# Performance work log

Measured on AMD Instinct MI355X. Metric: run time of the kernel, lower is better.

The kernel has to match this reference:

```python
import jax, jax.numpy as jnp
import numpy as np

B, S, D = 2, 4096, 1024
H, DK = 16, 64          # heads, QK feature dim per head
DV = D // H             # output features per head = 64
QKV_OUT = (2 * DK + DV) * H  # 3072


def setup_inputs() -> dict:
    key = jax.random.key(0)
    k1, k2, k3, k4, k5 = jax.random.split(key, 5)
    x = jax.random.normal(k1, (B, S, D), dtype=jnp.float32)
    Wqkv = jax.random.normal(k2, (D, QKV_OUT), dtype=jnp.float32) * (1.0 / np.sqrt(D))
    bqkv = jnp.zeros((QKV_OUT,), dtype=jnp.float32)
    Wproj = jax.random.normal(k3, (D, D), dtype=jnp.float32) * (1.0 / np.sqrt(D))
    bproj = jnp.zeros((D,), dtype=jnp.float32)
    return {"x": x, "Wqkv": Wqkv, "bqkv": bqkv, "Wproj": Wproj, "bproj": bproj}


def reference(x, Wqkv, bqkv, Wproj, bproj):
    # QKV projection: [B,S,(2*DK+DV)*H]
    qkv = x @ Wqkv + bqkv
    q_len = DK * H
    Q = qkv[:, :, :q_len].reshape(B, S, H, DK).transpose(0, 2, 1, 3)        # [B,H,S,DK]
    K = qkv[:, :, q_len:2 * q_len].reshape(B, S, H, DK).transpose(0, 2, 1, 3)
    V = qkv[:, :, 2 * q_len:].reshape(B, S, H, DV).transpose(0, 2, 1, 3)    # [B,H,S,DV]

    scores = jnp.einsum("bhqd,bhkd->bhqk", Q, K) * (1.0 / np.sqrt(DK))
    # Faithful to source: causal mask is tril(ones) with zeros -> -inf,
    # i.e. +1.0 is ADDED on allowed positions (harmless constant shift per row).
    tril = jnp.tril(jnp.ones((S, S), dtype=jnp.float32))
    mask = jnp.where(tril == 0, -jnp.inf, tril)
    scores = scores + mask
    attn = jax.nn.softmax(scores, axis=-1)  # dropout disabled (p=0 / eval)

    out = jnp.einsum("bhqk,bhkd->bhqd", attn, V)            # [B,H,S,DV]
    out = out.transpose(0, 2, 1, 3).reshape(B, S, H * DV)   # [B,S,D]
    return out @ Wproj + bproj
```

## Files before the change

kernel.cpp:

```cpp
#include <hip/hip_runtime.h>
#include <stdint.h>


typedef __bf16 bf16x8 __attribute__((ext_vector_type(8)));
typedef float f32x4 __attribute__((ext_vector_type(4)));
typedef unsigned short u16x8 __attribute__((ext_vector_type(8)));
typedef unsigned short u16x4 __attribute__((ext_vector_type(4)));
typedef unsigned int u32x4 __attribute__((ext_vector_type(4)));

__device__ __forceinline__ unsigned short f2bf(float f) {
  unsigned u = __builtin_bit_cast(unsigned, f);
  u += 0x7FFFu + ((u >> 16) & 1u);
  return (unsigned short)(u >> 16);
}

__device__ __forceinline__ float fast_exp2(float x) {
#if __has_builtin(__builtin_amdgcn_exp2f)
  return __builtin_amdgcn_exp2f(x);
#else
  return exp2f(x);
#endif
}

__device__ __forceinline__ void gload16(const void* g, void* l) {
  __builtin_amdgcn_global_load_lds(
      (__attribute__((address_space(1))) unsigned int*)(uintptr_t)g,
      (__attribute__((address_space(3))) unsigned int*)(unsigned int)(uintptr_t)l,
      16, 0, 0);
}

__global__ void k_cvt_bf16(const float* __restrict__ in,
                           unsigned short* __restrict__ out, int n8) {
  int i = blockIdx.x * blockDim.x + threadIdx.x;
  if (i >= n8) return;
  const float4* p = reinterpret_cast<const float4*>(in) + (size_t)i * 2;
  float4 a = p[0], b = p[1];
  u16x8 o;
  o[0] = f2bf(a.x); o[1] = f2bf(a.y); o[2] = f2bf(a.z); o[3] = f2bf(a.w);
  o[4] = f2bf(b.x); o[5] = f2bf(b.y); o[6] = f2bf(b.z); o[7] = f2bf(b.w);
  *(reinterpret_cast<u16x8*>(out) + i) = o;
}

__global__ void k_transcvt(const float* __restrict__ in,
                           unsigned short* __restrict__ out, int K, int N) {
  __shared__ float tile[32][33];
  int tk0 = blockIdx.y << 5, tn0 = blockIdx.x << 5;
  int t = threadIdx.x;
  int r = t >> 3, c4 = (t & 7) << 2;
  float4 v = *reinterpret_cast<const float4*>(&in[(size_t)(tk0 + r) * N + tn0 + c4]);
  tile[r][c4 + 0] = v.x; tile[r][c4 + 1] = v.y;
  tile[r][c4 + 2] = v.z; tile[r][c4 + 3] = v.w;
  __syncthreads();
  u16x4 o;
  o[0] = f2bf(tile[c4 + 0][r]); o[1] = f2bf(tile[c4 + 1][r]);
  o[2] = f2bf(tile[c4 + 2][r]); o[3] = f2bf(tile[c4 + 3][r]);
  *reinterpret_cast<u16x4*>(&out[(size_t)(tn0 + r) * K + tk0 + c4]) = o;
}

__global__ __launch_bounds__(512, 2) void k_gemm_qkv256(
    const unsigned short* __restrict__ A, const unsigned short* __restrict__ Bt,
    const float* __restrict__ bias, unsigned short* __restrict__ Qb,
    unsigned short* __restrict__ Kb, unsigned short* __restrict__ VTb) {
  __shared__ unsigned short Aring[4][8192];
  __shared__ unsigned short Bring[4][8192];
  const int t = threadIdx.x;
  const int lane = t & 63;
  const int w = t >> 6;
  const int wr = w >> 2, wc = w & 3;
  const int l15 = lane & 15, l4 = lane >> 4;
  const int m0 = blockIdx.y << 8, n0 = blockIdx.x << 8;

  const int ca0 = t, ca1 = t + 512;
  const size_t gA0 = (size_t)(m0 + (ca0 & 255)) * 1024 + ((ca0 >> 8) << 3);
  const size_t gA1 = (size_t)(m0 + (ca1 & 255)) * 1024 + ((ca1 >> 8) << 3);
  const size_t gB0 = (size_t)(n0 + (ca0 & 255)) * 1024 + ((ca0 >> 8) << 3);
  const size_t gB1 = (size_t)(n0 + (ca1 & 255)) * 1024 + ((ca1 >> 8) << 3);

  const int abase = l4 * 2048 + (wr * 128 + l15) * 8;
  const int bbase = l4 * 2048 + (wc * 64 + l15) * 8;

  f32x4 acc[8][4] = {};

  auto stageU = [&](int g) {
    const int s = g & 3;
    const int k = g << 5;
    gload16(A + gA0 + k, &Aring[s][ca0 * 8]);
    gload16(A + gA1 + k, &Aring[s][ca1 * 8]);
    gload16(Bt + gB0 + k, &Bring[s][ca0 * 8]);
    gload16(Bt + gB1 + k, &Bring[s][ca1 * 8]);
  };

  auto computeU = [&](int g, bool doStage) {
    const unsigned short* As = Aring[g & 3];
    const unsigned short* Bs = Bring[g & 3];
    bf16x8 bfr[4], af[4];
#pragma unroll
    for (int nf = 0; nf < 4; ++nf)
      bfr[nf] = *reinterpret_cast<const bf16x8*>(Bs + bbase + nf * 128);
#pragma unroll
    for (int mf = 0; mf < 4; ++mf)
      af[mf] = *reinterpret_cast<const bf16x8*>(As + abase + mf * 128);
    if (doStage) stageU(g + 3);
    __builtin_amdgcn_s_setprio(1);
#pragma unroll
    for (int mf = 0; mf < 4; ++mf)
#pragma unroll
      for (int nf = 0; nf < 4; ++nf)
        acc[mf][nf] = __builtin_amdgcn_mfma_f32_16x16x32_bf16(af[mf], bfr[nf],
                                                              acc[mf][nf], 0, 0, 0);
    __builtin_amdgcn_s_setprio(0);
#pragma unroll
    for (int mf = 0; mf < 4; ++mf)
      af[mf] = *reinterpret_cast<const bf16x8*>(As + abase + 512 + mf * 128);
    __builtin_amdgcn_s_setprio(1);
#pragma unroll
    for (int mf = 0; mf < 4; ++mf)
#pragma unroll
      for (int nf = 0; nf < 4; ++nf)
        acc[4 + mf][nf] = __builtin_amdgcn_mfma_f32_16x16x32_bf16(
            af[mf], bfr[nf], acc[4 + mf][nf], 0, 0, 0);
    __builtin_amdgcn_s_setprio(0);
  };

  stageU(0); stageU(1); stageU(2);
  asm volatile("s_waitcnt vmcnt(8)" ::: "memory");
  asm volatile("s_barrier" ::: "memory");

#pragma unroll 1
  for (int g = 0; g < 29; ++g) {
    computeU(g, true);
    asm volatile("s_waitcnt vmcnt(8)" ::: "memory");
    asm volatile("s_barrier" ::: "memory");
  }
  computeU(29, false);
  asm volatile("s_waitcnt vmcnt(4)" ::: "memory");
  asm volatile("s_barrier" ::: "memory");
  computeU(30, false);
  asm volatile("s_waitcnt vmcnt(0)" ::: "memory");
  asm volatile("s_barrier" ::: "memory");
  computeU(31, false);

  const float C1 = 0.18033688011112043f;
  float bi[4];
#pragma unroll
  for (int nf = 0; nf < 4; ++nf) bi[nf] = bias[n0 + wc * 64 + nf * 16 + l15];

  if (n0 < 1024) {
#pragma unroll
    for (int amf = 0; amf < 8; ++amf)
#pragma unroll
      for (int nf = 0; nf < 4; ++nf)
#pragma unroll
        for (int j = 0; j < 4; ++j) {
          int row = m0 + wr * 128 + amf * 16 + l4 * 4 + j;
          int col = n0 + wc * 64 + nf * 16 + l15;
          float v = (acc[amf][nf][j] + bi[nf]) * C1;
          int b = row >> 12, s = row & 4095;
          int hh = col >> 6, d = col & 63;
          Qb[((size_t)(b * 16 + hh) * 4096 + s) * 64 + d] = f2bf(v);
        }
  } else if (n0 < 2048) {
#pragma unroll
    for (int amf = 0; amf < 8; ++amf)
#pragma unroll
      for (int nf = 0; nf < 4; ++nf)
#pragma unroll
        for (int j = 0; j < 4; ++j) {
          int row = m0 + wr * 128 + amf * 16 + l4 * 4 + j;
          int cc = n0 - 1024 + wc * 64 + nf * 16 + l15;
          float v = acc[amf][nf][j] + bi[nf];
          int b = row >> 12, s = row & 4095;
          int hh = cc >> 6, d = cc & 63;
          Kb[((size_t)(b * 16 + hh) * 4096 + s) * 64 + d] = f2bf(v);
        }
  } else {
#pragma unroll
    for (int amf = 0; amf < 8; ++amf)
#pragma unroll
      for (int nf = 0; nf < 4; ++nf)
#pragma unroll
        for (int j = 0; j < 4; ++j) {
          int row = m0 + wr * 128 + amf * 16 + l4 * 4 + j;
          int cc = n0 - 2048 + wc * 64 + nf * 16 + l15;
          float v = acc[amf][nf][j] + bi[nf];
          int b = row >> 12, s = row & 4095;
          int hh = cc >> 6, d = cc & 63;
          VTb[((size_t)(b * 16 + hh) * 64 + d) * 4096 + s] = f2bf(v);
        }
  }
}

__device__ __forceinline__ void gemm_core(
    const unsigned short* __restrict__ A, const unsigned short* __restrict__ Bt,
    unsigned short* Al, unsigned short* Bl, int m0, int n0, f32x4 acc[4][4]) {
  const int t = threadIdx.x;
  const int lane = t & 63;
  const int w = t >> 6;
  const int wr = w >> 1, wc = w & 1;
  const int l15 = lane & 15, l4 = lane >> 4;

  const int c0 = t, c1 = t + 256;
  const int r0 = c0 >> 2, s0 = ((c0 & 3) << 3) ^ (((r0 >> 1) & 3) << 3);
  const int r1 = c1 >> 2, s1 = ((c1 & 3) << 3) ^ (((r1 >> 1) & 3) << 3);
  const size_t ga0 = (size_t)(m0 + r0) * 1024 + s0;
  const size_t ga1 = (size_t)(m0 + r1) * 1024 + s1;
  const size_t gb0 = (size_t)(n0 + r0) * 1024 + s0;
  const size_t gb1 = (size_t)(n0 + r1) * 1024 + s1;

  int aidx[4], bidx[4];
#pragma unroll
  for (int m = 0; m < 4; ++m) {
    int row = wr * 64 + m * 16 + l15;
    aidx[m] = row * 32 + ((l4 * 8) ^ (((row >> 1) & 3) << 3));
    row = wc * 64 + m * 16 + l15;
    bidx[m] = row * 32 + ((l4 * 8) ^ (((row >> 1) & 3) << 3));
  }

  for (int kk = 0; kk < 1024; kk += 32) {
    __syncthreads();
    gload16(A + ga0 + kk, Al + c0 * 8);
    gload16(A + ga1 + kk, Al + c1 * 8);
    gload16(Bt + gb0 + kk, Bl + c0 * 8);
    gload16(Bt + gb1 + kk, Bl + c1 * 8);
    __syncthreads();
    bf16x8 af[4], bfr[4];
#pragma unroll
    for (int m = 0; m < 4; ++m)
      af[m] = *reinterpret_cast<const bf16x8*>(Al + aidx[m]);
#pragma unroll
    for (int n = 0; n < 4; ++n)
      bfr[n] = *reinterpret_cast<const bf16x8*>(Bl + bidx[n]);
#pragma unroll
    for (int m = 0; m < 4; ++m)
#pragma unroll
      for (int n = 0; n < 4; ++n)
        acc[m][n] = __builtin_amdgcn_mfma_f32_16x16x32_bf16(af[m], bfr[n],
                                                            acc[m][n], 0, 0, 0);
  }
}

__global__ __launch_bounds__(256) void k_gemm_proj(
    const unsigned short* __restrict__ A, const unsigned short* __restrict__ Bt,
    const float* __restrict__ bias, float* __restrict__ out) {
  __shared__ unsigned short Al[128 * 32];
  __shared__ unsigned short Bl[128 * 32];
  const int lane = threadIdx.x & 63, w = threadIdx.x >> 6;
  const int wr = w >> 1, wc = w & 1;
  const int l15 = lane & 15, l4 = lane >> 4;
  const int m0 = blockIdx.y << 7, n0 = blockIdx.x << 7;

  f32x4 acc[4][4] = {};
  gemm_core(A, Bt, Al, Bl, m0, n0, acc);

#pragma unroll
  for (int m = 0; m < 4; ++m) {
#pragma unroll
    for (int n = 0; n < 4; ++n) {
#pragma unroll
      for (int j = 0; j < 4; ++j) {
        int row = m0 + wr * 64 + m * 16 + l4 * 4 + j;
        int col = n0 + wc * 64 + n * 16 + l15;
        out[(size_t)row * 1024 + col] = acc[m][n][j] + bias[col];
      }
    }
  }
}

__global__ __launch_bounds__(256, 4) void k_attn(
    const unsigned short* __restrict__ Qb, const unsigned short* __restrict__ Kb,
    const unsigned short* __restrict__ VTb, unsigned short* __restrict__ Ob) {
  __shared__ unsigned short Kl[2][64 * 64];
  __shared__ unsigned short Vl[2][64 * 64];
  const int t = threadIdx.x;
  const int lane = t & 63, w = t >> 6;
  const int l15 = lane & 15, l4 = lane >> 4;
  const int idx = blockIdx.x;
  const int qt = 31 - (idx >> 5);
  const int bh = idx & 31;
  const size_t qkbase = (size_t)bh * 4096 * 64;
  const size_t vbase = (size_t)bh * 64 * 4096;
  const int b = bh >> 4, hh = bh & 15;
  const int wrow0 = qt * 128 + w * 32;
  const int nt = 2 * qt + 2;

  const int c0 = t, c1 = t + 256;
  const int kr0 = c0 >> 3, ks0 = ((c0 & 7) << 3) ^ ((kr0 & 7) << 3);
  const int kr1 = c1 >> 3, ks1 = ((c1 & 7) << 3) ^ ((kr1 & 7) << 3);

#define STAGE(bufi, jt)                                                             \
  do {                                                                              \
    gload16(Kb + qkbase + (size_t)((jt) * 64 + kr0) * 64 + ks0, &Kl[bufi][c0 * 8]); \
    gload16(Kb + qkbase + (size_t)((jt) * 64 + kr1) * 64 + ks1, &Kl[bufi][c1 * 8]); \
    gload16(VTb + vbase + (size_t)kr0 * 4096 + (jt) * 64 + ks0, &Vl[bufi][c0 * 8]); \
    gload16(VTb + vbase + (size_t)kr1 * 4096 + (jt) * 64 + ks1, &Vl[bufi][c1 * 8]); \
  } while (0)

  bf16x8 qf[2][2];
#pragma unroll
  for (int m = 0; m < 2; ++m)
#pragma unroll
    for (int kk = 0; kk < 2; ++kk)
      qf[m][kk] = *reinterpret_cast<const bf16x8*>(
          &Qb[qkbase + (size_t)(wrow0 + m * 16 + l15) * 64 + kk * 32 + l4 * 8]);

  f32x4 oacc[2][4] = {};
  float lsum[2] = {};

  STAGE(0, 0);
  asm volatile("s_waitcnt vmcnt(0)" ::: "memory");
  __builtin_amdgcn_s_barrier();

  for (int j = 0; j < nt; ++j) {
    const int cur = j & 1;
    if (j + 1 < nt) STAGE(cur ^ 1, j + 1);

    const int jk0 = j * 64;
    const bool active = (jk0 <= wrow0 + 31);
    const bool needmask = active && (jk0 + 63 > wrow0);

    if (active) {
#pragma unroll
      for (int h = 0; h < 2; ++h) {
        f32x4 sch[2][2] = {};
        __builtin_amdgcn_s_setprio(1);
#pragma unroll
        for (int nn = 0; nn < 2; ++nn) {
          int krow = (h * 2 + nn) * 16 + l15;
#pragma unroll
          for (int kk = 0; kk < 2; ++kk) {
            int kcol = (kk * 32 + l4 * 8) ^ ((krow & 7) << 3);
            bf16x8 kfr = *reinterpret_cast<const bf16x8*>(&Kl[cur][krow * 64 + kcol]);
#pragma unroll
            for (int m = 0; m < 2; ++m)
              sch[m][nn] = __builtin_amdgcn_mfma_f32_16x16x32_bf16(
                  kfr, qf[m][kk], sch[m][nn], 0, 0, 0);
          }
        }
        __builtin_amdgcn_s_setprio(0);

        bf16x8 pa[2];
#pragma unroll
        for (int m = 0; m < 2; ++m) {
#pragma unroll
          for (int nn = 0; nn < 2; ++nn)
#pragma unroll
            for (int r = 0; r < 4; ++r)
              sch[m][nn][r] = fast_exp2(sch[m][nn][r]);
          if (needmask) {
            const int qg = wrow0 + m * 16 + l15;
#pragma unroll
            for (int nn = 0; nn < 2; ++nn) {
              const int kb = jk0 + (h * 2 + nn) * 16 + l4 * 4;
#pragma unroll
              for (int r = 0; r < 4; ++r)
                if (kb + r > qg) sch[m][nn][r] = 0.f;
            }
          }
#pragma unroll
          for (int nn = 0; nn < 2; ++nn)
#pragma unroll
            for (int r = 0; r < 4; ++r)
              lsum[m] += sch[m][nn][r];

          unsigned A0, A1, B0, B1;
          asm("v_cvt_pk_bf16_f32 %0, %1, %2"
              : "=v"(A0) : "v"(sch[m][0][0]), "v"(sch[m][0][1]));
          asm("v_cvt_pk_bf16_f32 %0, %1, %2"
              : "=v"(A1) : "v"(sch[m][0][2]), "v"(sch[m][0][3]));
          asm("v_cvt_pk_bf16_f32 %0, %1, %2"
              : "=v"(B0) : "v"(sch[m][1][0]), "v"(sch[m][1][1]));
          asm("v_cvt_pk_bf16_f32 %0, %1, %2"
              : "=v"(B1) : "v"(sch[m][1][2]), "v"(sch[m][1][3]));
          asm("v_permlane32_swap_b32 %0, %1" : "+v"(A0), "+v"(B0));
          asm("v_permlane16_swap_b32 %0, %1" : "+v"(A0), "+v"(B0));
          asm("v_permlane32_swap_b32 %0, %1" : "+v"(A1), "+v"(B1));
          asm("v_permlane16_swap_b32 %0, %1" : "+v"(A1), "+v"(B1));
          u32x4 pw;
          pw[0] = A0; pw[1] = A1; pw[2] = B0; pw[3] = B1;
          pa[m] = __builtin_bit_cast(bf16x8, pw);
        }

        __builtin_amdgcn_s_setprio(1);
#pragma unroll
        for (int nn2 = 0; nn2 < 4; ++nn2) {
          int vr = nn2 * 16 + l15;
          int vc = (h * 32 + l4 * 8) ^ ((vr & 7) << 3);
          bf16x8 vf = *reinterpret_cast<const bf16x8*>(&Vl[cur][vr * 64 + vc]);
          oacc[0][nn2] = __builtin_amdgcn_mfma_f32_16x16x32_bf16(
              pa[0], vf, oacc[0][nn2], 0, 0, 0);
          oacc[1][nn2] = __builtin_amdgcn_mfma_f32_16x16x32_bf16(
              pa[1], vf, oacc[1][nn2], 0, 0, 0);
        }
        __builtin_amdgcn_s_setprio(0);
      }
    }

    asm volatile("s_waitcnt vmcnt(0)" ::: "memory");
    __builtin_amdgcn_s_barrier();
  }
#undef STAGE

#pragma unroll
  for (int m = 0; m < 2; ++m) {
    lsum[m] += __shfl_xor(lsum[m], 16);
    lsum[m] += __shfl_xor(lsum[m], 32);
  }
#pragma unroll
  for (int m = 0; m < 2; ++m)
#pragma unroll
    for (int jj = 0; jj < 4; ++jj) {
      float inv = 1.0f / __shfl(lsum[m], l4 * 4 + jj);
      int srow = wrow0 + m * 16 + l4 * 4 + jj;
#pragma unroll
      for (int nn = 0; nn < 4; ++nn) {
        int col = hh * 64 + nn * 16 + l15;
        Ob[((size_t)(b * 4096 + srow)) * 1024 + col] =
            __builtin_bit_cast(unsigned short, (__bf16)(oacc[m][nn][jj] * inv));
      }
    }
}

extern "C" void kernel_launch(void* const* d_in, const int* in_sizes, int n_in,
                              void* d_out, int out_size, void* d_ws, size_t ws_size,
                              hipStream_t stream) {
  const float* x = (const float*)d_in[0];
  const float* Wqkv = (const float*)d_in[1];
  const float* bqkv = (const float*)d_in[2];
  const float* Wproj = (const float*)d_in[3];
  const float* bproj = (const float*)d_in[4];

  char* ws = (char*)d_ws;
  unsigned short* xb  = (unsigned short*)(ws);
  unsigned short* Wqb = (unsigned short*)(ws + 16777216);
  unsigned short* Wpb = (unsigned short*)(ws + 23068672);
  unsigned short* Qb  = (unsigned short*)(ws + 25165824);
  unsigned short* Kb  = (unsigned short*)(ws + 41943040);
  unsigned short* VTb = (unsigned short*)(ws + 58720256);
  unsigned short* Ob  = (unsigned short*)(ws + 75497472);

  k_cvt_bf16<<<dim3(8388608 / 8 / 256), dim3(256), 0, stream>>>(x, xb, 8388608 / 8);
  k_transcvt<<<dim3(3072 / 32, 1024 / 32), dim3(256), 0, stream>>>(Wqkv, Wqb, 1024, 3072);
  k_transcvt<<<dim3(1024 / 32, 1024 / 32), dim3(256), 0, stream>>>(Wproj, Wpb, 1024, 1024);
  k_gemm_qkv256<<<dim3(3072 / 256, 8192 / 256), dim3(512), 0, stream>>>(xb, Wqb, bqkv, Qb, Kb, VTb);
  k_attn<<<dim3(1024), dim3(256), 0, stream>>>(Qb, Kb, VTb, Ob);
  k_gemm_proj<<<dim3(1024 / 128, 8192 / 128), dim3(256), 0, stream>>>(Ob, Wpb, bproj, (float*)d_out);
}
```

Measured before the change: 232.7 us.

## Swizzle QKV GEMM block order and split K-step into two barrier-synced phases

The QKV GEMM launch becomes a 1D grid of 384 blocks, remapped so that consecutive block IDs are spread by XCD (bid&7) across M/N tiles, aiming for better L2 locality of shared A/B tiles per chiplet. The main loop is restructured into two phases per K-step: A prefetch is issued in the first phase and B prefetch in the second, each bracketed by barriers, sched_barrier and priority raises so MFMA groups across waves line up and global loads are split. This adds extra barriers per iteration and uses a separate register set for the second A half, which could raise register pressure.

After: 225.5 us. -3.1%, faster.

```diff
diff --git a/kernel.cpp b/kernel.cpp
--- a/kernel.cpp
+++ b/kernel.cpp
@@ -68,7 +68,10 @@
   const int w = t >> 6;
   const int wr = w >> 2, wc = w & 3;
   const int l15 = lane & 15, l4 = lane >> 4;
-  const int m0 = blockIdx.y << 8, n0 = blockIdx.x << 8;
+
+  const int bid = blockIdx.x;
+  const int swz = (bid & 7) * 48 + (bid >> 3);
+  const int n0 = (swz % 12) << 8, m0 = (swz / 12) << 8;
 
   const int ca0 = t, ca1 = t + 512;
   const size_t gA0 = (size_t)(m0 + (ca0 & 255)) * 1024 + ((ca0 >> 8) << 3);
@@ -81,16 +84,32 @@
 
   f32x4 acc[8][4] = {};
 
-  auto stageU = [&](int g) {
-    const int s = g & 3;
-    const int k = g << 5;
+  auto stageA = [&](int g) {
+    const int s = g & 3, k = g << 5;
     gload16(A + gA0 + k, &Aring[s][ca0 * 8]);
     gload16(A + gA1 + k, &Aring[s][ca1 * 8]);
+  };
+  auto stageB = [&](int g) {
+    const int s = g & 3, k = g << 5;
     gload16(Bt + gB0 + k, &Bring[s][ca0 * 8]);
     gload16(Bt + gB1 + k, &Bring[s][ca1 * 8]);
   };
 
-  auto computeU = [&](int g, bool doStage) {
+#define PHASE_TAIL                                  \
+  asm volatile("s_barrier" ::: "memory");           \
+  __builtin_amdgcn_sched_barrier(0);                \
+  __builtin_amdgcn_s_setprio(1);
+
+#define PHASE_END                                   \
+  __builtin_amdgcn_s_setprio(0);                    \
+  asm volatile("s_barrier" ::: "memory");
+
+  stageA(0); stageB(0); stageA(1); stageB(1); stageA(2); stageB(2);
+  asm volatile("s_waitcnt vmcnt(8)" ::: "memory");
+  asm volatile("s_barrier" ::: "memory");
+
+#pragma unroll 1
+  for (int g = 0; g < 32; ++g) {
     const unsigned short* As = Aring[g & 3];
     const unsigned short* Bs = Bring[g & 3];
     bf16x8 bfr[4], af[4];
@@ -100,45 +119,38 @@
 #pragma unroll
     for (int mf = 0; mf < 4; ++mf)
       af[mf] = *reinterpret_cast<const bf16x8*>(As + abase + mf * 128);
-    if (doStage) stageU(g + 3);
-    __builtin_amdgcn_s_setprio(1);
+    if (g < 29) stageA(g + 3);
+    PHASE_TAIL
 #pragma unroll
     for (int mf = 0; mf < 4; ++mf)
 #pragma unroll
       for (int nf = 0; nf < 4; ++nf)
         acc[mf][nf] = __builtin_amdgcn_mfma_f32_16x16x32_bf16(af[mf], bfr[nf],
                                                               acc[mf][nf], 0, 0, 0);
-    __builtin_amdgcn_s_setprio(0);
+    PHASE_END
+    bf16x8 ah[4];
 #pragma unroll
     for (int mf = 0; mf < 4; ++mf)
-      af[mf] = *reinterpret_cast<const bf16x8*>(As + abase + 512 + mf * 128);
-    __builtin_amdgcn_s_setprio(1);
+      ah[mf] = *reinterpret_cast<const bf16x8*>(As + abase + 512 + mf * 128);
+    if (g < 29) {
+      stageB(g + 3);
+      asm volatile("s_waitcnt vmcnt(8)" ::: "memory");
+    } else if (g == 29) {
+      asm volatile("s_waitcnt vmcnt(4)" ::: "memory");
+    } else if (g == 30) {
+      asm volatile("s_waitcnt vmcnt(0)" ::: "memory");
+    }
+    PHASE_TAIL
 #pragma unroll
     for (int mf = 0; mf < 4; ++mf)
 #pragma unroll
       for (int nf = 0; nf < 4; ++nf)
         acc[4 + mf][nf] = __builtin_amdgcn_mfma_f32_16x16x32_bf16(
-            af[mf], bfr[nf], acc[4 + mf][nf], 0, 0, 0);
-    __builtin_amdgcn_s_setprio(0);
-  };
-
-  stageU(0); stageU(1); stageU(2);
-  asm volatile("s_waitcnt vmcnt(8)" ::: "memory");
-  asm volatile("s_barrier" ::: "memory");
-
-#pragma unroll 1
-  for (int g = 0; g < 29; ++g) {
-    computeU(g, true);
-    asm volatile("s_waitcnt vmcnt(8)" ::: "memory");
-    asm volatile("s_barrier" ::: "memory");
-  }
-  computeU(29, false);
-  asm volatile("s_waitcnt vmcnt(4)" ::: "memory");
-  asm volatile("s_barrier" ::: "memory");
-  computeU(30, false);
-  asm volatile("s_waitcnt vmcnt(0)" ::: "memory");
-  asm volatile("s_barrier" ::: "memory");
-  computeU(31, false);
+            ah[mf], bfr[nf], acc[4 + mf][nf], 0, 0, 0);
+    PHASE_END
+  }
+#undef PHASE_TAIL
+#undef PHASE_END
 
   const float C1 = 0.18033688011112043f;
   float bi[4];
@@ -441,7 +453,7 @@
   k_cvt_bf16<<<dim3(8388608 / 8 / 256), dim3(256), 0, stream>>>(x, xb, 8388608 / 8);
   k_transcvt<<<dim3(3072 / 32, 1024 / 32), dim3(256), 0, stream>>>(Wqkv, Wqb, 1024, 3072);
   k_transcvt<<<dim3(1024 / 32, 1024 / 32), dim3(256), 0, stream>>>(Wproj, Wpb, 1024, 1024);
-  k_gemm_qkv256<<<dim3(3072 / 256, 8192 / 256), dim3(512), 0, stream>>>(xb, Wqb, bqkv, Qb, Kb, VTb);
+  k_gemm_qkv256<<<dim3(384), dim3(512), 0, stream>>>(xb, Wqb, bqkv, Qb, Kb, VTb);
   k_attn<<<dim3(1024), dim3(256), 0, stream>>>(Qb, Kb, VTb, Ob);
   k_gemm_proj<<<dim3(1024 / 128, 8192 / 128), dim3(256), 0, stream>>>(Ob, Wpb, bproj, (float*)d_out);
 }
```
